# Kernel tuning notes

Measured on AMD Instinct MI355X. Metric: run time of the kernel, lower is better.

Reference implementation:

```python
import jax, jax.numpy as jnp
import numpy as np

GOP = 4

def _resize_bilinear(x, Ho, Wo):
    # x: (M, C, Hs, Ws); matches F.interpolate(mode='bilinear', align_corners=False)
    M, C, Hs, Ws = x.shape
    ys = jnp.clip((jnp.arange(Ho, dtype=jnp.float32) + 0.5) * (Hs / Ho) - 0.5, 0.0, Hs - 1.0)
    xs = jnp.clip((jnp.arange(Wo, dtype=jnp.float32) + 0.5) * (Ws / Wo) - 0.5, 0.0, Ws - 1.0)
    y0 = jnp.floor(ys).astype(jnp.int32); y1 = jnp.minimum(y0 + 1, Hs - 1)
    x0 = jnp.floor(xs).astype(jnp.int32); x1 = jnp.minimum(x0 + 1, Ws - 1)
    wy = (ys - y0)[None, None, :, None]
    wx = (xs - x0)[None, None, None, :]
    r0 = x[:, :, y0, :]; r1 = x[:, :, y1, :]
    top = r0[:, :, :, x0] * (1 - wx) + r0[:, :, :, x1] * wx
    bot = r1[:, :, :, x0] * (1 - wx) + r1[:, :, :, x1] * wx
    return top * (1 - wy) + bot * wy

def _deform_sample(feat, flow):
    # feat: (M,C,H,W); flow: (M,2,H,W), ch0=dy, ch1=dx (torchvision deform_conv order).
    # Bilinear sample at (y+dy, x+dx) with zero padding outside (kernel_size=1 deform conv).
    M, C, H, W = feat.shape
    gy = jnp.arange(H, dtype=flow.dtype)[:, None]
    gx = jnp.arange(W, dtype=flow.dtype)[None, :]
    y = gy + flow[:, 0]; x = gx + flow[:, 1]          # (M,H,W)
    y0f = jnp.floor(y); x0f = jnp.floor(x)
    wy = (y - y0f)[:, None]; wx = (x - x0f)[:, None]  # (M,1,H,W)
    y0 = y0f.astype(jnp.int32); x0 = x0f.astype(jnp.int32)
    feat_flat = feat.reshape(M, C, H * W)
    def gather(yi, xi):
        valid = ((yi >= 0) & (yi < H) & (xi >= 0) & (xi < W)).astype(feat.dtype)
        idx = (jnp.clip(yi, 0, H - 1) * W + jnp.clip(xi, 0, W - 1)).reshape(M, H * W)
        v = jnp.take_along_axis(feat_flat, jnp.broadcast_to(idx[:, None, :], (M, C, H * W)), axis=2)
        return v.reshape(M, C, H, W) * valid[:, None]
    v00 = gather(y0, x0);     v01 = gather(y0, x0 + 1)
    v10 = gather(y0 + 1, x0); v11 = gather(y0 + 1, x0 + 1)
    return v00 * (1 - wy) * (1 - wx) + v01 * (1 - wy) * wx + v10 * wy * (1 - wx) + v11 * wy * wx

def setup_inputs():
    key = jax.random.key(0)
    k = jax.random.split(key, 7)
    B, T, Himg, Wimg = 4, 16, 256, 256
    num_gop = T // GOP      # 4
    t = GOP - 1             # 3 P-frames per GOP
    C_in, D, h, w = 256, 256, 64, 64
    imgs = jnp.zeros((B, T, 3, Himg, Wimg), jnp.float32)
    i_features = jax.random.normal(k[0], (B * num_gop, C_in, h, w), jnp.float32)
    # flows of a few pixels at image scale (scaled by 0.25 inside forward)
    p_motions = jax.random.normal(k[1], (B, num_gop * t, 2, Himg, Wimg), jnp.float32) * 8.0
    W_emb = jax.random.normal(k[2], (D, C_in), jnp.float32) * 0.02
    b_emb = jax.random.normal(k[3], (D,), jnp.float32) * 0.02
    W_dc = jax.random.normal(k[4], (D, D), jnp.float32) * 0.02
    b_dc = jax.random.normal(k[5], (D,), jnp.float32) * 0.02
    return {"imgs": imgs, "i_features": i_features, "p_motions": p_motions,
            "W_emb": W_emb, "b_emb": b_emb, "W_dc": W_dc, "b_dc": b_dc}

def reference(imgs, i_features, p_motions, W_emb, b_emb, W_dc, b_dc):
    B = imgs.shape[0]
    num_gop = imgs.shape[1] // GOP
    # 1x1 embedding conv
    feat = jnp.einsum('mchw,oc->mohw', i_features, W_emb) + b_emb[None, :, None, None]
    M0, D, h, w = feat.shape
    scale = w / imgs.shape[-1]
    Tp = p_motions.shape[1]
    flow = _resize_bilinear(p_motions.reshape(B * Tp, 2, p_motions.shape[-2], p_motions.shape[-1]), h, w) * scale
    t = Tp // num_gop
    # repeat each GOP's I-frame features for its t P-frame flows
    feat = jnp.broadcast_to(feat.reshape(B, num_gop, 1, D, h, w), (B, num_gop, t, D, h, w)).reshape(-1, D, h, w)
    flow = flow.reshape(-1, 2, h, w)
    # flow-guided deformable conv with 1x1 kernel: bilinear gather + 1x1 projection
    samp = _deform_sample(feat, flow)
    out = jnp.einsum('mchw,oc->mohw', samp, W_dc) + b_dc[None, :, None, None]
    # adaptive_avg_pool2d(.,1).flatten(3)
    return out.mean(axis=(-2, -1)).reshape(B, num_gop, t, D)
```

## Files before the change

kernel.cpp:

```cpp
#include <hip/hip_runtime.h>
#include <math.h>

#define HW 4096
#define CIN 256
#define DD 256
#define M_TOTAL 48
#define NSP 4
#define SPPX (HW / NSP)

__global__ __launch_bounds__(256) void k_flow_scatter(
    const float* __restrict__ p_motions,
    float* __restrict__ Ag,
    float* __restrict__ Sg)
{
    __shared__ float Al[HW];
    __shared__ float red[4];
    const int m = blockIdx.x;
    const int sp = blockIdx.y;
    const int tid = threadIdx.x;
    const float* p0 = p_motions + (size_t)m * 2 * 65536;
    const float* p1 = p0 + 65536;

    for (int i = tid; i < HW; i += 256) Al[i] = 0.f;
    __syncthreads();

    for (int ii = tid; ii < SPPX; ii += 256) {
        const int i = sp * SPPX + ii;
        const int y = i >> 6, x = i & 63;
        const int r1 = 4 * y + 1, r2 = 4 * y + 2;
        const int c1 = 4 * x + 1, c2 = 4 * x + 2;
        float a = p0[r1 * 256 + c1], b = p0[r1 * 256 + c2];
        float c = p0[r2 * 256 + c1], d = p0[r2 * 256 + c2];
        float fy = ((a * 0.5f + b * 0.5f) * 0.5f + (c * 0.5f + d * 0.5f) * 0.5f) * 0.25f;
        a = p1[r1 * 256 + c1]; b = p1[r1 * 256 + c2];
        c = p1[r2 * 256 + c1]; d = p1[r2 * 256 + c2];
        float fx = ((a * 0.5f + b * 0.5f) * 0.5f + (c * 0.5f + d * 0.5f) * 0.5f) * 0.25f;

        const float yy = (float)y + fy;
        const float xx = (float)x + fx;
        const float y0f = floorf(yy), x0f = floorf(xx);
        const float wy = yy - y0f, wx = xx - x0f;
        const int iy0 = (int)y0f, ix0 = (int)x0f;
        const int iy1 = iy0 + 1, ix1 = ix0 + 1;
        const float w00 = (1.f - wy) * (1.f - wx);
        const float w01 = (1.f - wy) * wx;
        const float w10 = wy * (1.f - wx);
        const float w11 = wy * wx;
        const bool y0ok = (iy0 >= 0) & (iy0 < 64);
        const bool y1ok = (iy1 >= 0) & (iy1 < 64);
        const bool x0ok = (ix0 >= 0) & (ix0 < 64);
        const bool x1ok = (ix1 >= 0) & (ix1 < 64);
        if (y0ok & x0ok) atomicAdd(&Al[iy0 * 64 + ix0], w00);
        if (y0ok & x1ok) atomicAdd(&Al[iy0 * 64 + ix1], w01);
        if (y1ok & x0ok) atomicAdd(&Al[iy1 * 64 + ix0], w10);
        if (y1ok & x1ok) atomicAdd(&Al[iy1 * 64 + ix1], w11);
    }
    __syncthreads();

    float part = 0.f;
    float* AgM = Ag + (size_t)m * HW;
    for (int i = tid; i < HW; i += 256) {
        const float v = Al[i];
        part += v;
        if (v != 0.f) atomicAdd(&AgM[i], v);
    }
    for (int off = 32; off > 0; off >>= 1) part += __shfl_down(part, off, 64);
    const int wave = tid >> 6, lane = tid & 63;
    if (lane == 0) red[wave] = part;
    __syncthreads();
    if (tid == 0) atomicAdd(&Sg[m], red[0] + red[1] + red[2] + red[3]);
}

__global__ __launch_bounds__(256) void k_fold(
    const float* __restrict__ W_emb,
    const float* __restrict__ b_emb,
    const float* __restrict__ W_dc,
    float* __restrict__ WT,
    float* __restrict__ bfold)
{
    __shared__ float wdc[256];
    __shared__ float red[4];
    const int o = blockIdx.x, tid = threadIdx.x;
    wdc[tid] = W_dc[(size_t)o * 256 + tid];
    __syncthreads();
    float acc = 0.f;
    #pragma unroll 8
    for (int k = 0; k < 256; ++k)
        acc += wdc[k] * W_emb[(size_t)k * 256 + tid];
    WT[(size_t)tid * 256 + o] = acc;

    float pb = wdc[tid] * b_emb[tid];
    for (int off = 32; off > 0; off >>= 1) pb += __shfl_down(pb, off, 64);
    if ((tid & 63) == 0) red[tid >> 6] = pb;
    __syncthreads();
    if (tid == 0) bfold[o] = red[0] + red[1] + red[2] + red[3];
}

__global__ __launch_bounds__(256) void k_gather_dot(
    const float* __restrict__ i_features,
    const float* __restrict__ Ag,
    float* __restrict__ gpart)
{
    __shared__ float Al[3][SPPX];
    const int fm = blockIdx.x;
    const int chunk = blockIdx.y;
    const int sp = blockIdx.z;
    const int tid = threadIdx.x;
    const int m0 = fm * 3;

    {
        const float4* s0 = (const float4*)(Ag + (size_t)(m0 + 0) * HW + sp * SPPX);
        const float4* s1 = (const float4*)(Ag + (size_t)(m0 + 1) * HW + sp * SPPX);
        const float4* s2 = (const float4*)(Ag + (size_t)(m0 + 2) * HW + sp * SPPX);
        ((float4*)Al[0])[tid] = s0[tid];
        ((float4*)Al[1])[tid] = s1[tid];
        ((float4*)Al[2])[tid] = s2[tid];
    }
    __syncthreads();

    const int wave = tid >> 6, lane = tid & 63;
    const float4* A0 = (const float4*)Al[0];
    const float4* A1 = (const float4*)Al[1];
    const float4* A2 = (const float4*)Al[2];

    for (int cl = wave; cl < 16; cl += 4) {
        const int ci = chunk * 16 + cl;
        const float4* f4 = (const float4*)(i_features + ((size_t)fm * CIN + ci) * HW + sp * SPPX);
        float s0 = 0.f, s1 = 0.f, s2 = 0.f;
        #pragma unroll
        for (int k = lane; k < SPPX / 4; k += 64) {
            const float4 v = f4[k];
            const float4 a0 = A0[k], a1 = A1[k], a2 = A2[k];
            s0 += v.x * a0.x + v.y * a0.y + v.z * a0.z + v.w * a0.w;
            s1 += v.x * a1.x + v.y * a1.y + v.z * a1.z + v.w * a1.w;
            s2 += v.x * a2.x + v.y * a2.y + v.z * a2.z + v.w * a2.w;
        }
        for (int off = 32; off > 0; off >>= 1) {
            s0 += __shfl_down(s0, off, 64);
            s1 += __shfl_down(s1, off, 64);
            s2 += __shfl_down(s2, off, 64);
        }
        if (lane == 0) {
            gpart[((size_t)sp * M_TOTAL + m0 + 0) * CIN + ci] = s0;
            gpart[((size_t)sp * M_TOTAL + m0 + 1) * CIN + ci] = s1;
            gpart[((size_t)sp * M_TOTAL + m0 + 2) * CIN + ci] = s2;
        }
    }
}

__global__ __launch_bounds__(256) void k_out(
    const float* __restrict__ gpart,
    const float* __restrict__ Sg,
    const float* __restrict__ WT,
    const float* __restrict__ bfold,
    const float* __restrict__ b_dc,
    float* __restrict__ out)
{
    __shared__ float gl[CIN];
    const int m = blockIdx.x;
    const int tid = threadIdx.x;

    float gv = 0.f;
    for (int sp = 0; sp < NSP; ++sp)
        gv += gpart[((size_t)sp * M_TOTAL + m) * CIN + tid];
    gl[tid] = gv * (1.f / 4096.f);
    __syncthreads();

    const float Sm = Sg[m] * (1.f / 4096.f);
    float acc = 0.f;
    #pragma unroll 8
    for (int ci = 0; ci < CIN; ++ci)
        acc += gl[ci] * WT[(size_t)ci * DD + tid];
    out[(size_t)m * DD + tid] = acc + bfold[tid] * Sm + b_dc[tid];
}

extern "C" void kernel_launch(void* const* d_in, const int* in_sizes, int n_in,
                              void* d_out, int out_size, void* d_ws, size_t ws_size,
                              hipStream_t stream) {
    const float* i_features = (const float*)d_in[1];
    const float* p_motions  = (const float*)d_in[2];
    const float* W_emb      = (const float*)d_in[3];
    const float* b_emb      = (const float*)d_in[4];
    const float* W_dc       = (const float*)d_in[5];
    const float* b_dc       = (const float*)d_in[6];
    float* out = (float*)d_out;

    float* ws = (float*)d_ws;
    float* Ag    = ws;
    float* Sg    = Ag + (size_t)M_TOTAL * HW;
    float* WT    = Sg + 64;
    float* bfold = WT + 65536;
    float* gpart = bfold + 256;

    hipMemsetAsync(Ag, 0, ((size_t)M_TOTAL * HW + 64) * sizeof(float), stream);

    dim3 g1(M_TOTAL, NSP);
    k_flow_scatter<<<g1, 256, 0, stream>>>(p_motions, Ag, Sg);
    k_fold<<<DD, 256, 0, stream>>>(W_emb, b_emb, W_dc, WT, bfold);
    dim3 g3(16, 16, NSP);
    k_gather_dot<<<g3, 256, 0, stream>>>(i_features, Ag, gpart);
    k_out<<<M_TOTAL, 256, 0, stream>>>(gpart, Sg, WT, bfold, b_dc, out);
}
```

Measured before the change: 172.0 us.

## Merge flow scatter and weight transpose into one kernel, drop memset and fold GEMM

Combines the flow scatter and weight preparation into a single prologue kernel. Each sample's full 4096-pixel scatter now runs in one 1024-thread block, so results are stored directly instead of accumulated with global atomics, and the memset is removed. The 256x256x256 weight-fold matmul is replaced by plain transposes, with both projections applied sequentially in the output kernel. The gather-dot kernel keeps the scatter weights in registers rather than shared memory. This cuts launches and the fold GEMM work, at the cost of a second 256x256 matvec per sample in the output kernel and higher register pressure.

```diff
diff --git a/kernel.cpp b/kernel.cpp
--- a/kernel.cpp
+++ b/kernel.cpp
@@ -8,133 +8,125 @@
 #define NSP 4
 #define SPPX (HW / NSP)
 
-__global__ __launch_bounds__(256) void k_flow_scatter(
+__global__ __launch_bounds__(1024) void k_pre(
     const float* __restrict__ p_motions,
+    const float* __restrict__ W_emb,
+    const float* __restrict__ W_dc,
     float* __restrict__ Ag,
-    float* __restrict__ Sg)
+    float* __restrict__ Sg,
+    float* __restrict__ WembT,
+    float* __restrict__ WdcT)
 {
-    __shared__ float Al[HW];
-    __shared__ float red[4];
-    const int m = blockIdx.x;
-    const int sp = blockIdx.y;
+    __shared__ float smem[64 * 65];
     const int tid = threadIdx.x;
-    const float* p0 = p_motions + (size_t)m * 2 * 65536;
-    const float* p1 = p0 + 65536;
-
-    for (int i = tid; i < HW; i += 256) Al[i] = 0.f;
-    __syncthreads();
-
-    for (int ii = tid; ii < SPPX; ii += 256) {
-        const int i = sp * SPPX + ii;
-        const int y = i >> 6, x = i & 63;
-        const int r1 = 4 * y + 1, r2 = 4 * y + 2;
-        const int c1 = 4 * x + 1, c2 = 4 * x + 2;
-        float a = p0[r1 * 256 + c1], b = p0[r1 * 256 + c2];
-        float c = p0[r2 * 256 + c1], d = p0[r2 * 256 + c2];
-        float fy = ((a * 0.5f + b * 0.5f) * 0.5f + (c * 0.5f + d * 0.5f) * 0.5f) * 0.25f;
-        a = p1[r1 * 256 + c1]; b = p1[r1 * 256 + c2];
-        c = p1[r2 * 256 + c1]; d = p1[r2 * 256 + c2];
-        float fx = ((a * 0.5f + b * 0.5f) * 0.5f + (c * 0.5f + d * 0.5f) * 0.5f) * 0.25f;
-
-        const float yy = (float)y + fy;
-        const float xx = (float)x + fx;
-        const float y0f = floorf(yy), x0f = floorf(xx);
-        const float wy = yy - y0f, wx = xx - x0f;
-        const int iy0 = (int)y0f, ix0 = (int)x0f;
-        const int iy1 = iy0 + 1, ix1 = ix0 + 1;
-        const float w00 = (1.f - wy) * (1.f - wx);
-        const float w01 = (1.f - wy) * wx;
-        const float w10 = wy * (1.f - wx);
-        const float w11 = wy * wx;
-        const bool y0ok = (iy0 >= 0) & (iy0 < 64);
-        const bool y1ok = (iy1 >= 0) & (iy1 < 64);
-        const bool x0ok = (ix0 >= 0) & (ix0 < 64);
-        const bool x1ok = (ix1 >= 0) & (ix1 < 64);
-        if (y0ok & x0ok) atomicAdd(&Al[iy0 * 64 + ix0], w00);
-        if (y0ok & x1ok) atomicAdd(&Al[iy0 * 64 + ix1], w01);
-        if (y1ok & x0ok) atomicAdd(&Al[iy1 * 64 + ix0], w10);
-        if (y1ok & x1ok) atomicAdd(&Al[iy1 * 64 + ix1], w11);
+    const int bid = blockIdx.x;
+
+    if (bid < M_TOTAL) {
+        __shared__ float Ssum;
+        const int m = bid;
+        const float* p0 = p_motions + (size_t)m * 2 * 65536;
+        const float* p1 = p0 + 65536;
+
+        for (int i = tid; i < HW; i += 1024) smem[i] = 0.f;
+        if (tid == 0) Ssum = 0.f;
+        __syncthreads();
+
+        for (int i = tid; i < HW; i += 1024) {
+            const int y = i >> 6, x = i & 63;
+            const int r1 = 4 * y + 1, r2 = 4 * y + 2;
+            const int c1 = 4 * x + 1, c2 = 4 * x + 2;
+            float a = p0[r1 * 256 + c1], b = p0[r1 * 256 + c2];
+            float c = p0[r2 * 256 + c1], d = p0[r2 * 256 + c2];
+            float fy = (a + b + c + d) * 0.0625f;
+            a = p1[r1 * 256 + c1]; b = p1[r1 * 256 + c2];
+            c = p1[r2 * 256 + c1]; d = p1[r2 * 256 + c2];
+            float fx = (a + b + c + d) * 0.0625f;
+
+            const float yy = (float)y + fy;
+            const float xx = (float)x + fx;
+            const float y0f = floorf(yy), x0f = floorf(xx);
+            const float wy = yy - y0f, wx = xx - x0f;
+            const int iy0 = (int)y0f, ix0 = (int)x0f;
+            const int iy1 = iy0 + 1, ix1 = ix0 + 1;
+            const float w00 = (1.f - wy) * (1.f - wx);
+            const float w01 = (1.f - wy) * wx;
+            const float w10 = wy * (1.f - wx);
+            const float w11 = wy * wx;
+            const bool y0ok = (iy0 >= 0) & (iy0 < 64);
+            const bool y1ok = (iy1 >= 0) & (iy1 < 64);
+            const bool x0ok = (ix0 >= 0) & (ix0 < 64);
+            const bool x1ok = (ix1 >= 0) & (ix1 < 64);
+            if (y0ok & x0ok) atomicAdd(&smem[iy0 * 64 + ix0], w00);
+            if (y0ok & x1ok) atomicAdd(&smem[iy0 * 64 + ix1], w01);
+            if (y1ok & x0ok) atomicAdd(&smem[iy1 * 64 + ix0], w10);
+            if (y1ok & x1ok) atomicAdd(&smem[iy1 * 64 + ix1], w11);
+        }
+        __syncthreads();
+
+        float part = 0.f;
+        float* AgM = Ag + (size_t)m * HW;
+        for (int i = tid; i < HW; i += 1024) {
+            const float v = smem[i];
+            AgM[i] = v;
+            part += v;
+        }
+        for (int off = 32; off > 0; off >>= 1) part += __shfl_down(part, off, 64);
+        if ((tid & 63) == 0) atomicAdd(&Ssum, part);
+        __syncthreads();
+        if (tid == 0) Sg[m] = Ssum;
+    } else {
+        const int t = bid - M_TOTAL;
+        const float* src = (t < 16) ? W_emb : W_dc;
+        float* dst       = (t < 16) ? WembT : WdcT;
+        const int tt = t & 15;
+        const int bi = tt >> 2, bj = tt & 3;
+        const int w = tid >> 6, lane = tid & 63;
+        float (*Ld)[65] = (float (*)[65])smem;
+
+        for (int r = w; r < 64; r += 16)
+            Ld[r][lane] = src[(size_t)(bi * 64 + r) * 256 + bj * 64 + lane];
+        __syncthreads();
+        for (int r = w; r < 64; r += 16)
+            dst[(size_t)(bj * 64 + r) * 256 + bi * 64 + lane] = Ld[lane][r];
     }
-    __syncthreads();
-
-    float part = 0.f;
-    float* AgM = Ag + (size_t)m * HW;
-    for (int i = tid; i < HW; i += 256) {
-        const float v = Al[i];
-        part += v;
-        if (v != 0.f) atomicAdd(&AgM[i], v);
-    }
-    for (int off = 32; off > 0; off >>= 1) part += __shfl_down(part, off, 64);
-    const int wave = tid >> 6, lane = tid & 63;
-    if (lane == 0) red[wave] = part;
-    __syncthreads();
-    if (tid == 0) atomicAdd(&Sg[m], red[0] + red[1] + red[2] + red[3]);
-}
-
-__global__ __launch_bounds__(256) void k_fold(
-    const float* __restrict__ W_emb,
-    const float* __restrict__ b_emb,
-    const float* __restrict__ W_dc,
-    float* __restrict__ WT,
-    float* __restrict__ bfold)
-{
-    __shared__ float wdc[256];
-    __shared__ float red[4];
-    const int o = blockIdx.x, tid = threadIdx.x;
-    wdc[tid] = W_dc[(size_t)o * 256 + tid];
-    __syncthreads();
-    float acc = 0.f;
-    #pragma unroll 8
-    for (int k = 0; k < 256; ++k)
-        acc += wdc[k] * W_emb[(size_t)k * 256 + tid];
-    WT[(size_t)tid * 256 + o] = acc;
-
-    float pb = wdc[tid] * b_emb[tid];
-    for (int off = 32; off > 0; off >>= 1) pb += __shfl_down(pb, off, 64);
-    if ((tid & 63) == 0) red[tid >> 6] = pb;
-    __syncthreads();
-    if (tid == 0) bfold[o] = red[0] + red[1] + red[2] + red[3];
-}
-
-__global__ __launch_bounds__(256) void k_gather_dot(
+}
+
+__global__ __launch_bounds__(256, 4) void k_gather_dot(
     const float* __restrict__ i_features,
     const float* __restrict__ Ag,
     float* __restrict__ gpart)
 {
-    __shared__ float Al[3][SPPX];
     const int fm = blockIdx.x;
     const int chunk = blockIdx.y;
     const int sp = blockIdx.z;
     const int tid = threadIdx.x;
+    const int wave = tid >> 6, lane = tid & 63;
     const int m0 = fm * 3;
 
-    {
-        const float4* s0 = (const float4*)(Ag + (size_t)(m0 + 0) * HW + sp * SPPX);
-        const float4* s1 = (const float4*)(Ag + (size_t)(m0 + 1) * HW + sp * SPPX);
-        const float4* s2 = (const float4*)(Ag + (size_t)(m0 + 2) * HW + sp * SPPX);
-        ((float4*)Al[0])[tid] = s0[tid];
-        ((float4*)Al[1])[tid] = s1[tid];
-        ((float4*)Al[2])[tid] = s2[tid];
+    const float4* A0 = (const float4*)(Ag + (size_t)(m0 + 0) * HW + sp * SPPX);
+    const float4* A1 = (const float4*)(Ag + (size_t)(m0 + 1) * HW + sp * SPPX);
+    const float4* A2 = (const float4*)(Ag + (size_t)(m0 + 2) * HW + sp * SPPX);
+    float4 a0[4], a1[4], a2[4];
+    #pragma unroll
+    for (int k = 0; k < 4; ++k) {
+        a0[k] = A0[lane + 64 * k];
+        a1[k] = A1[lane + 64 * k];
+        a2[k] = A2[lane + 64 * k];
     }
-    __syncthreads();
-
-    const int wave = tid >> 6, lane = tid & 63;
-    const float4* A0 = (const float4*)Al[0];
-    const float4* A1 = (const float4*)Al[1];
-    const float4* A2 = (const float4*)Al[2];
-
-    for (int cl = wave; cl < 16; cl += 4) {
-        const int ci = chunk * 16 + cl;
+
+    #pragma unroll
+    for (int c = 0; c < 4; ++c) {
+        const int ci = chunk * 16 + wave * 4 + c;
         const float4* f4 = (const float4*)(i_features + ((size_t)fm * CIN + ci) * HW + sp * SPPX);
         float s0 = 0.f, s1 = 0.f, s2 = 0.f;
         #pragma unroll
-        for (int k = lane; k < SPPX / 4; k += 64) {
-            const float4 v = f4[k];
-            const float4 a0 = A0[k], a1 = A1[k], a2 = A2[k];
-            s0 += v.x * a0.x + v.y * a0.y + v.z * a0.z + v.w * a0.w;
-            s1 += v.x * a1.x + v.y * a1.y + v.z * a1.z + v.w * a1.w;
-            s2 += v.x * a2.x + v.y * a2.y + v.z * a2.z + v.w * a2.w;
-        }
+        for (int k = 0; k < 4; ++k) {
+            const float4 v = f4[lane + 64 * k];
+            s0 += v.x * a0[k].x + v.y * a0[k].y + v.z * a0[k].z + v.w * a0[k].w;
+            s1 += v.x * a1[k].x + v.y * a1[k].y + v.z * a1[k].z + v.w * a1[k].w;
+            s2 += v.x * a2[k].x + v.y * a2[k].y + v.z * a2[k].z + v.w * a2[k].w;
+        }
+        #pragma unroll
         for (int off = 32; off > 0; off >>= 1) {
             s0 += __shfl_down(s0, off, 64);
             s1 += __shfl_down(s1, off, 64);
@@ -151,12 +143,14 @@
 __global__ __launch_bounds__(256) void k_out(
     const float* __restrict__ gpart,
     const float* __restrict__ Sg,
-    const float* __restrict__ WT,
-    const float* __restrict__ bfold,
+    const float* __restrict__ WembT,
+    const float* __restrict__ WdcT,
+    const float* __restrict__ b_emb,
     const float* __restrict__ b_dc,
     float* __restrict__ out)
 {
     __shared__ float gl[CIN];
+    __shared__ float sm[DD];
     const int m = blockIdx.x;
     const int tid = threadIdx.x;
 
@@ -169,9 +163,16 @@
     const float Sm = Sg[m] * (1.f / 4096.f);
     float acc = 0.f;
     #pragma unroll 8
-    for (int ci = 0; ci < CIN; ++ci)
-        acc += gl[ci] * WT[(size_t)ci * DD + tid];
-    out[(size_t)m * DD + tid] = acc + bfold[tid] * Sm + b_dc[tid];
+    for (int c = 0; c < CIN; ++c)
+        acc += gl[c] * WembT[(size_t)c * DD + tid];
+    sm[tid] = acc + b_emb[tid] * Sm;
+    __syncthreads();
+
+    float acc2 = 0.f;
+    #pragma unroll 8
+    for (int k = 0; k < DD; ++k)
+        acc2 += sm[k] * WdcT[(size_t)k * DD + tid];
+    out[(size_t)m * DD + tid] = acc2 + b_dc[tid];
 }
 
 extern "C" void kernel_launch(void* const* d_in, const int* in_sizes, int n_in,
@@ -188,16 +189,13 @@
     float* ws = (float*)d_ws;
     float* Ag    = ws;
     float* Sg    = Ag + (size_t)M_TOTAL * HW;
-    float* WT    = Sg + 64;
-    float* bfold = WT + 65536;
-    float* gpart = bfold + 256;
-
-    hipMemsetAsync(Ag, 0, ((size_t)M_TOTAL * HW + 64) * sizeof(float), stream);
-
-    dim3 g1(M_TOTAL, NSP);
-    k_flow_scatter<<<g1, 256, 0, stream>>>(p_motions, Ag, Sg);
-    k_fold<<<DD, 256, 0, stream>>>(W_emb, b_emb, W_dc, WT, bfold);
-    dim3 g3(16, 16, NSP);
-    k_gather_dot<<<g3, 256, 0, stream>>>(i_features, Ag, gpart);
-    k_out<<<M_TOTAL, 256, 0, stream>>>(gpart, Sg, WT, bfold, b_dc, out);
-}
+    float* WembT = Sg + 64;
+    float* WdcT  = WembT + 65536;
+    float* gpart = WdcT + 65536;
+
+    k_pre<<<M_TOTAL + 32, 1024, 0, stream>>>(p_motions, W_emb, W_dc,
+                                             Ag, Sg, WembT, WdcT);
+    dim3 g2(16, 16, NSP);
+    k_gather_dot<<<g2, 256, 0, stream>>>(i_features, Ag, gpart);
+    k_out<<<M_TOTAL, 256, 0, stream>>>(gpart, Sg, WembT, WdcT, b_emb, b_dc, out);
+}
```

Measured after the change: 183.2 us. 1.06x slower.

## Merge flow scatter and weight fold into one launch; keep flow weights in registers

Applied to the files above, without the earlier changes.

Combines the flow-scatter and weight-folding kernels into a single launch whose blocks split by index. This removes one launch and lets the two independent jobs run at the same time. The flow downsample now reads float4 rows with simplified arithmetic. The gather-dot kernel loads its scatter weights straight into registers instead of staging them through shared memory with a barrier, and it fully unrolls the channel loop with a launch-bounds occupancy hint. The combined kernel sizes its shared memory for the larger branch, which may reduce how many blocks fit per CU.

```diff
diff --git a/kernel.cpp b/kernel.cpp
--- a/kernel.cpp
+++ b/kernel.cpp
@@ -8,133 +8,131 @@
 #define NSP 4
 #define SPPX (HW / NSP)
 
-__global__ __launch_bounds__(256) void k_flow_scatter(
+__global__ __launch_bounds__(256) void k_pre(
     const float* __restrict__ p_motions,
-    float* __restrict__ Ag,
-    float* __restrict__ Sg)
-{
-    __shared__ float Al[HW];
-    __shared__ float red[4];
-    const int m = blockIdx.x;
-    const int sp = blockIdx.y;
-    const int tid = threadIdx.x;
-    const float* p0 = p_motions + (size_t)m * 2 * 65536;
-    const float* p1 = p0 + 65536;
-
-    for (int i = tid; i < HW; i += 256) Al[i] = 0.f;
-    __syncthreads();
-
-    for (int ii = tid; ii < SPPX; ii += 256) {
-        const int i = sp * SPPX + ii;
-        const int y = i >> 6, x = i & 63;
-        const int r1 = 4 * y + 1, r2 = 4 * y + 2;
-        const int c1 = 4 * x + 1, c2 = 4 * x + 2;
-        float a = p0[r1 * 256 + c1], b = p0[r1 * 256 + c2];
-        float c = p0[r2 * 256 + c1], d = p0[r2 * 256 + c2];
-        float fy = ((a * 0.5f + b * 0.5f) * 0.5f + (c * 0.5f + d * 0.5f) * 0.5f) * 0.25f;
-        a = p1[r1 * 256 + c1]; b = p1[r1 * 256 + c2];
-        c = p1[r2 * 256 + c1]; d = p1[r2 * 256 + c2];
-        float fx = ((a * 0.5f + b * 0.5f) * 0.5f + (c * 0.5f + d * 0.5f) * 0.5f) * 0.25f;
-
-        const float yy = (float)y + fy;
-        const float xx = (float)x + fx;
-        const float y0f = floorf(yy), x0f = floorf(xx);
-        const float wy = yy - y0f, wx = xx - x0f;
-        const int iy0 = (int)y0f, ix0 = (int)x0f;
-        const int iy1 = iy0 + 1, ix1 = ix0 + 1;
-        const float w00 = (1.f - wy) * (1.f - wx);
-        const float w01 = (1.f - wy) * wx;
-        const float w10 = wy * (1.f - wx);
-        const float w11 = wy * wx;
-        const bool y0ok = (iy0 >= 0) & (iy0 < 64);
-        const bool y1ok = (iy1 >= 0) & (iy1 < 64);
-        const bool x0ok = (ix0 >= 0) & (ix0 < 64);
-        const bool x1ok = (ix1 >= 0) & (ix1 < 64);
-        if (y0ok & x0ok) atomicAdd(&Al[iy0 * 64 + ix0], w00);
-        if (y0ok & x1ok) atomicAdd(&Al[iy0 * 64 + ix1], w01);
-        if (y1ok & x0ok) atomicAdd(&Al[iy1 * 64 + ix0], w10);
-        if (y1ok & x1ok) atomicAdd(&Al[iy1 * 64 + ix1], w11);
-    }
-    __syncthreads();
-
-    float part = 0.f;
-    float* AgM = Ag + (size_t)m * HW;
-    for (int i = tid; i < HW; i += 256) {
-        const float v = Al[i];
-        part += v;
-        if (v != 0.f) atomicAdd(&AgM[i], v);
-    }
-    for (int off = 32; off > 0; off >>= 1) part += __shfl_down(part, off, 64);
-    const int wave = tid >> 6, lane = tid & 63;
-    if (lane == 0) red[wave] = part;
-    __syncthreads();
-    if (tid == 0) atomicAdd(&Sg[m], red[0] + red[1] + red[2] + red[3]);
-}
-
-__global__ __launch_bounds__(256) void k_fold(
     const float* __restrict__ W_emb,
     const float* __restrict__ b_emb,
     const float* __restrict__ W_dc,
+    float* __restrict__ Ag,
+    float* __restrict__ Sg,
     float* __restrict__ WT,
     float* __restrict__ bfold)
 {
-    __shared__ float wdc[256];
-    __shared__ float red[4];
-    const int o = blockIdx.x, tid = threadIdx.x;
-    wdc[tid] = W_dc[(size_t)o * 256 + tid];
-    __syncthreads();
-    float acc = 0.f;
-    #pragma unroll 8
-    for (int k = 0; k < 256; ++k)
-        acc += wdc[k] * W_emb[(size_t)k * 256 + tid];
-    WT[(size_t)tid * 256 + o] = acc;
-
-    float pb = wdc[tid] * b_emb[tid];
-    for (int off = 32; off > 0; off >>= 1) pb += __shfl_down(pb, off, 64);
-    if ((tid & 63) == 0) red[tid >> 6] = pb;
-    __syncthreads();
-    if (tid == 0) bfold[o] = red[0] + red[1] + red[2] + red[3];
-}
-
-__global__ __launch_bounds__(256) void k_gather_dot(
+    const int tid = threadIdx.x;
+    const int bid = blockIdx.x;
+
+    if (bid < M_TOTAL * NSP) {
+        __shared__ float Al[HW];
+        __shared__ float red[4];
+        const int m = bid >> 2;
+        const int sp = bid & 3;
+        const float4* p0 = (const float4*)(p_motions + (size_t)m * 2 * 65536);
+        const float4* p1 = p0 + 65536 / 4;
+
+        for (int i = tid; i < HW; i += 256) Al[i] = 0.f;
+        __syncthreads();
+
+        #pragma unroll
+        for (int ii = 0; ii < SPPX / 256; ++ii) {
+            const int i = ii * 256 + tid;
+            const int y = sp * 16 + (i >> 6);
+            const int x = i & 63;
+            const int r1 = 4 * y + 1, r2 = 4 * y + 2;
+            const float4 v10 = p0[r1 * 64 + x];
+            const float4 v20 = p0[r2 * 64 + x];
+            const float4 v11 = p1[r1 * 64 + x];
+            const float4 v21 = p1[r2 * 64 + x];
+            const float fy = (v10.y + v10.z + v20.y + v20.z) * 0.0625f;
+            const float fx = (v11.y + v11.z + v21.y + v21.z) * 0.0625f;
+
+            const float yy = (float)y + fy;
+            const float xx = (float)x + fx;
+            const float y0f = floorf(yy), x0f = floorf(xx);
+            const float wy = yy - y0f, wx = xx - x0f;
+            const int iy0 = (int)y0f, ix0 = (int)x0f;
+            const int iy1 = iy0 + 1, ix1 = ix0 + 1;
+            const float w00 = (1.f - wy) * (1.f - wx);
+            const float w01 = (1.f - wy) * wx;
+            const float w10 = wy * (1.f - wx);
+            const float w11 = wy * wx;
+            const bool y0ok = (iy0 >= 0) & (iy0 < 64);
+            const bool y1ok = (iy1 >= 0) & (iy1 < 64);
+            const bool x0ok = (ix0 >= 0) & (ix0 < 64);
+            const bool x1ok = (ix1 >= 0) & (ix1 < 64);
+            if (y0ok & x0ok) atomicAdd(&Al[iy0 * 64 + ix0], w00);
+            if (y0ok & x1ok) atomicAdd(&Al[iy0 * 64 + ix1], w01);
+            if (y1ok & x0ok) atomicAdd(&Al[iy1 * 64 + ix0], w10);
+            if (y1ok & x1ok) atomicAdd(&Al[iy1 * 64 + ix1], w11);
+        }
+        __syncthreads();
+
+        float part = 0.f;
+        float* AgM = Ag + (size_t)m * HW;
+        for (int i = tid; i < HW; i += 256) {
+            const float v = Al[i];
+            part += v;
+            if (v != 0.f) atomicAdd(&AgM[i], v);
+        }
+        for (int off = 32; off > 0; off >>= 1) part += __shfl_down(part, off, 64);
+        if ((tid & 63) == 0) red[tid >> 6] = part;
+        __syncthreads();
+        if (tid == 0) atomicAdd(&Sg[m], red[0] + red[1] + red[2] + red[3]);
+    } else {
+        __shared__ float wdc[256];
+        __shared__ float red2[4];
+        const int o = bid - M_TOTAL * NSP;
+        wdc[tid] = W_dc[(size_t)o * 256 + tid];
+        __syncthreads();
+        float acc = 0.f;
+        #pragma unroll 8
+        for (int k = 0; k < 256; ++k)
+            acc += wdc[k] * W_emb[(size_t)k * 256 + tid];
+        WT[(size_t)tid * 256 + o] = acc;
+
+        float pb = wdc[tid] * b_emb[tid];
+        for (int off = 32; off > 0; off >>= 1) pb += __shfl_down(pb, off, 64);
+        if ((tid & 63) == 0) red2[tid >> 6] = pb;
+        __syncthreads();
+        if (tid == 0) bfold[o] = red2[0] + red2[1] + red2[2] + red2[3];
+    }
+}
+
+__global__ __launch_bounds__(256, 4) void k_gather_dot(
     const float* __restrict__ i_features,
     const float* __restrict__ Ag,
     float* __restrict__ gpart)
 {
-    __shared__ float Al[3][SPPX];
     const int fm = blockIdx.x;
     const int chunk = blockIdx.y;
     const int sp = blockIdx.z;
     const int tid = threadIdx.x;
+    const int wave = tid >> 6, lane = tid & 63;
     const int m0 = fm * 3;
 
-    {
-        const float4* s0 = (const float4*)(Ag + (size_t)(m0 + 0) * HW + sp * SPPX);
-        const float4* s1 = (const float4*)(Ag + (size_t)(m0 + 1) * HW + sp * SPPX);
-        const float4* s2 = (const float4*)(Ag + (size_t)(m0 + 2) * HW + sp * SPPX);
-        ((float4*)Al[0])[tid] = s0[tid];
-        ((float4*)Al[1])[tid] = s1[tid];
-        ((float4*)Al[2])[tid] = s2[tid];
+    const float4* A0 = (const float4*)(Ag + (size_t)(m0 + 0) * HW + sp * SPPX);
+    const float4* A1 = (const float4*)(Ag + (size_t)(m0 + 1) * HW + sp * SPPX);
+    const float4* A2 = (const float4*)(Ag + (size_t)(m0 + 2) * HW + sp * SPPX);
+    float4 a0[4], a1[4], a2[4];
+    #pragma unroll
+    for (int k = 0; k < 4; ++k) {
+        a0[k] = A0[lane + 64 * k];
+        a1[k] = A1[lane + 64 * k];
+        a2[k] = A2[lane + 64 * k];
     }
-    __syncthreads();
-
-    const int wave = tid >> 6, lane = tid & 63;
-    const float4* A0 = (const float4*)Al[0];
-    const float4* A1 = (const float4*)Al[1];
-    const float4* A2 = (const float4*)Al[2];
-
-    for (int cl = wave; cl < 16; cl += 4) {
-        const int ci = chunk * 16 + cl;
+
+    #pragma unroll
+    for (int c = 0; c < 4; ++c) {
+        const int ci = chunk * 16 + wave * 4 + c;
         const float4* f4 = (const float4*)(i_features + ((size_t)fm * CIN + ci) * HW + sp * SPPX);
         float s0 = 0.f, s1 = 0.f, s2 = 0.f;
         #pragma unroll
-        for (int k = lane; k < SPPX / 4; k += 64) {
-            const float4 v = f4[k];
-            const float4 a0 = A0[k], a1 = A1[k], a2 = A2[k];
-            s0 += v.x * a0.x + v.y * a0.y + v.z * a0.z + v.w * a0.w;
-            s1 += v.x * a1.x + v.y * a1.y + v.z * a1.z + v.w * a1.w;
-            s2 += v.x * a2.x + v.y * a2.y + v.z * a2.z + v.w * a2.w;
-        }
+        for (int k = 0; k < 4; ++k) {
+            const float4 v = f4[lane + 64 * k];
+            s0 += v.x * a0[k].x + v.y * a0[k].y + v.z * a0[k].z + v.w * a0[k].w;
+            s1 += v.x * a1[k].x + v.y * a1[k].y + v.z * a1[k].z + v.w * a1[k].w;
+            s2 += v.x * a2[k].x + v.y * a2[k].y + v.z * a2[k].z + v.w * a2[k].w;
+        }
+        #pragma unroll
         for (int off = 32; off > 0; off >>= 1) {
             s0 += __shfl_down(s0, off, 64);
             s1 += __shfl_down(s1, off, 64);
@@ -194,10 +192,9 @@
 
     hipMemsetAsync(Ag, 0, ((size_t)M_TOTAL * HW + 64) * sizeof(float), stream);
 
-    dim3 g1(M_TOTAL, NSP);
-    k_flow_scatter<<<g1, 256, 0, stream>>>(p_motions, Ag, Sg);
-    k_fold<<<DD, 256, 0, stream>>>(W_emb, b_emb, W_dc, WT, bfold);
-    dim3 g3(16, 16, NSP);
-    k_gather_dot<<<g3, 256, 0, stream>>>(i_features, Ag, gpart);
+    k_pre<<<M_TOTAL * NSP + DD, 256, 0, stream>>>(p_motions, W_emb, b_emb, W_dc,
+                                                  Ag, Sg, WT, bfold);
+    dim3 g2(16, 16, NSP);
+    k_gather_dot<<<g2, 256, 0, stream>>>(i_features, Ag, gpart);
     k_out<<<M_TOTAL, 256, 0, stream>>>(gpart, Sg, WT, bfold, b_dc, out);
 }
```

Measured after the change: 170.3 us. Within noise of the previous version (-1.0%).
